# Kernel optimization log

Measured on AMD Instinct MI355X. Metric: run time of the kernel, lower is better.

The kernel has to match this reference:

```python
import jax, jax.numpy as jnp
import numpy as np
from jax.ops import segment_sum

N_NODES = 100000


def gcn_conv(x, W, b, src, dst, num_nodes):
    # PyG GCNConv: h = x @ W; add self-loops; symmetric normalization; aggregate; + bias
    h = x @ W  # [N, out]
    # add self-loops
    loops = jnp.arange(num_nodes, dtype=src.dtype)
    src_sl = jnp.concatenate([src, loops])
    dst_sl = jnp.concatenate([dst, loops])
    # degree over destination (incl. self-loops), edge weight = 1
    deg = segment_sum(jnp.ones_like(src_sl, dtype=h.dtype), dst_sl, num_segments=num_nodes)
    dinv = jnp.where(deg > 0, jax.lax.rsqrt(deg), 0.0)
    norm = dinv[src_sl] * dinv[dst_sl]  # [E+N]
    msg = h[src_sl] * norm[:, None]      # gather + scale, [E+N, out]
    out = segment_sum(msg, dst_sl, num_segments=num_nodes)  # scatter-add
    return out + b


def setup_inputs() -> dict:
    key = jax.random.key(0)
    ks = jax.random.split(key, 5)
    N, F, C = N_NODES, 64, 10
    E = 1600000
    x = jax.random.normal(ks[0], (N, F), dtype=jnp.float32)
    edge_index = jax.random.randint(ks[1], (2, E), 0, N, dtype=jnp.int64)
    W1 = jax.random.normal(ks[2], (F, 128), dtype=jnp.float32) * (1.0 / np.sqrt(F))
    b1 = jnp.zeros((128,), dtype=jnp.float32)
    W2 = jax.random.normal(ks[3], (128, 16), dtype=jnp.float32) * (1.0 / np.sqrt(128))
    b2 = jnp.zeros((16,), dtype=jnp.float32)
    Wl = jax.random.normal(ks[4], (16, C), dtype=jnp.float32) * (1.0 / np.sqrt(16))
    bl = jnp.zeros((C,), dtype=jnp.float32)
    return {"x": x, "edge_index": edge_index, "W1": W1, "b1": b1,
            "W2": W2, "b2": b2, "Wl": Wl, "bl": bl}


def reference(x, edge_index, W1, b1, W2, b2, Wl, bl):
    src, dst = edge_index[0], edge_index[1]
    h = gcn_conv(x, W1, b1, src, dst, N_NODES)
    h = jax.nn.relu(h)
    h = gcn_conv(h, W2, b2, src, dst, N_NODES)
    h = jax.nn.relu(h)
    return h @ Wl + bl
```

## Files before the change

### kernel.cpp

```cpp
#include <hip/hip_runtime.h>
#include <hip/hip_fp16.h>


#define F_IN 64
#define H1DIM 128
#define H2DIM 16
#define C_OUT 10

#define NBK 1024
#define BSZ_LOG 7
#define BNODES 128
#define CAP 2816
#define SRC_BITS 17

typedef _Float16 f16x8 __attribute__((ext_vector_type(8)));
typedef _Float16 f16x4 __attribute__((ext_vector_type(4)));
typedef float f32x4 __attribute__((ext_vector_type(4)));

__global__ __launch_bounds__(256) void setup_kernel(
        const float* __restrict__ W1, const float* __restrict__ W2,
        f16x8* __restrict__ W1p, f16x8* __restrict__ W2p,
        int* __restrict__ cur) {
    int s = blockIdx.x * 256 + threadIdx.x;
    if (s < 1024) {
        int frag = s >> 6, lane = s & 63;
        int tile = frag >> 1, kf = frag & 1;
        int c = lane & 15, g = lane >> 4;
        f16x8 v;
#pragma unroll
        for (int j = 0; j < 8; ++j)
            v[j] = (_Float16)W1[(kf * 32 + g * 8 + j) * H1DIM + tile * 16 + c];
        W1p[s] = v;
    } else if (s < 1024 + 256) {
        int s2 = s - 1024;
        int f = s2 >> 6, lane = s2 & 63;
        int c = lane & 15, g = lane >> 4;
        f16x8 v;
#pragma unroll
        for (int j = 0; j < 8; ++j)
            v[j] = (_Float16)W2[(f * 32 + g * 8 + j) * H2DIM + c];
        W2p[s2] = v;
    } else {
        int t = s - 1280;
        if (t >= 0 && t < NBK) cur[t] = t * CAP;
    }
}

__global__ __launch_bounds__(256) void bucket_scatter(
        const int* __restrict__ ei, int E, int N,
        int* __restrict__ cursor, unsigned* __restrict__ pairs) {
    __shared__ int cnt[NBK];
    __shared__ int base[NBK];
    for (int t = threadIdx.x; t < NBK; t += 256) cnt[t] = 0;
    __syncthreads();

    const int4* s4 = (const int4*)ei;
    const int4* d4 = (const int4*)(ei + E);
    int chunk4 = blockIdx.x * 1024;
    int s_[16], d_[16];
    int m = 0;
#pragma unroll
    for (int r = 0; r < 4; r++) {
        int i4 = chunk4 + r * 256 + threadIdx.x;
        if (i4 * 4 < E) {
            int4 sv = s4[i4], dv = d4[i4];
            int ss[4] = {sv.x, sv.y, sv.z, sv.w};
            int dd[4] = {dv.x, dv.y, dv.z, dv.w};
#pragma unroll
            for (int q = 0; q < 4; q++) {
                if ((unsigned)ss[q] < (unsigned)N && (unsigned)dd[q] < (unsigned)N) {
                    s_[m] = ss[q]; d_[m] = dd[q]; m++;
                }
            }
        }
    }
    for (int k = 0; k < m; k++) atomicAdd(&cnt[d_[k] >> BSZ_LOG], 1);
    __syncthreads();
    for (int t = threadIdx.x; t < NBK; t += 256) {
        int c = cnt[t];
        base[t] = c ? atomicAdd(&cursor[t], c) : 0;
        cnt[t] = 0;
    }
    __syncthreads();
    for (int k = 0; k < m; k++) {
        int b = d_[k] >> BSZ_LOG;
        int pos = base[b] + atomicAdd(&cnt[b], 1);
        if (pos < (b + 1) * CAP)
            pairs[pos] = ((unsigned)(d_[k] & (BNODES - 1)) << SRC_BITS) | (unsigned)s_[k];
    }
}

__global__ __launch_bounds__(256) void build_csr_convert(
        const unsigned* __restrict__ pairs, const int* __restrict__ cursor,
        const float* __restrict__ x, int N,
        float* __restrict__ dinv, int* __restrict__ row_beg,
        int* __restrict__ row_end, int* __restrict__ csr_src,
        __half2* __restrict__ xh2) {
    int b = blockIdx.x;
    int base_node = b << BSZ_LOG;
    int nn = min(BNODES, N - base_node);
    __shared__ unsigned lp[CAP];
    __shared__ int cnt[BNODES];
    __shared__ int sc[BNODES];
    __shared__ int cur[BNODES];
    __shared__ float sdi[BNODES];
    int tid = threadIdx.x;
    if (tid < BNODES) cnt[tid] = 0;

    int pbeg = b * CAP;
    int pend = min(cursor[b], (b + 1) * CAP);
    int np = pend - pbeg;
    for (int j = tid; j < np; j += 256) lp[j] = pairs[pbeg + j];
    __syncthreads();

    for (int j = tid; j < np; j += 256)
        atomicAdd(&cnt[lp[j] >> SRC_BITS], 1);
    __syncthreads();

    int v = (tid < BNODES) ? cnt[tid] : 0;
    if (tid < BNODES) sc[tid] = v;
    __syncthreads();
#pragma unroll
    for (int off = 1; off < BNODES; off <<= 1) {
        int t = (tid < BNODES && tid >= off) ? sc[tid - off] : 0;
        __syncthreads();
        if (tid < BNODES) sc[tid] += t;
        __syncthreads();
    }
    if (tid < nn) {
        int ro = pbeg + sc[tid] - v;
        row_beg[base_node + tid] = ro;
        row_end[base_node + tid] = ro + v;
        cur[tid] = ro;
        float di = rsqrtf((float)(v + 1));
        dinv[base_node + tid] = di;
        sdi[tid] = di;
    }
    __syncthreads();

    for (int j = tid; j < np; j += 256) {
        unsigned p = lp[j];
        int dl = p >> SRC_BITS, s = p & ((1u << SRC_BITS) - 1);
        int pos = atomicAdd(&cur[dl], 1);
        csr_src[pos] = s;
    }

    const float2* x2 = (const float2*)x;
    int total = nn * 32;
    for (int t = tid; t < total; t += 256) {
        int nl = t >> 5, l = t & 31;
        float di = sdi[nl];
        long long idx = (long long)(base_node + nl) * 32 + l;
        float2 xv = x2[idx];
        xh2[idx] = __floats2half2_rn(xv.x * di, xv.y * di);
    }
}

__global__ __launch_bounds__(256) void gather1_h2(
        const f16x8* __restrict__ xh8, const float* __restrict__ dinv,
        const int* __restrict__ row_beg, const int* __restrict__ row_end,
        const int* __restrict__ csr_src, int N, f16x8* __restrict__ agg1h8) {
    int node = (blockIdx.x * 256 + threadIdx.x) >> 3;
    if (node >= N) return;
    int p = threadIdx.x & 7;
    int beg = row_beg[node], end = row_end[node];
    f16x8 self = xh8[(size_t)node * 8 + p];
    float acc[8];
#pragma unroll
    for (int q = 0; q < 8; q++) acc[q] = (float)self[q];
    int j = beg;
    for (; j + 8 <= end; j += 8) {
        int s0 = csr_src[j],     s1 = csr_src[j + 1];
        int s2 = csr_src[j + 2], s3 = csr_src[j + 3];
        int s4 = csr_src[j + 4], s5 = csr_src[j + 5];
        int s6 = csr_src[j + 6], s7 = csr_src[j + 7];
        f16x8 v0 = xh8[(size_t)s0 * 8 + p];
        f16x8 v1 = xh8[(size_t)s1 * 8 + p];
        f16x8 v2 = xh8[(size_t)s2 * 8 + p];
        f16x8 v3 = xh8[(size_t)s3 * 8 + p];
        f16x8 v4 = xh8[(size_t)s4 * 8 + p];
        f16x8 v5 = xh8[(size_t)s5 * 8 + p];
        f16x8 v6 = xh8[(size_t)s6 * 8 + p];
        f16x8 v7 = xh8[(size_t)s7 * 8 + p];
#pragma unroll
        for (int q = 0; q < 8; q++)
            acc[q] += (((float)v0[q] + (float)v1[q]) + ((float)v2[q] + (float)v3[q]))
                    + (((float)v4[q] + (float)v5[q]) + ((float)v6[q] + (float)v7[q]));
    }
    for (; j + 4 <= end; j += 4) {
        int s0 = csr_src[j], s1 = csr_src[j + 1];
        int s2 = csr_src[j + 2], s3 = csr_src[j + 3];
        f16x8 v0 = xh8[(size_t)s0 * 8 + p];
        f16x8 v1 = xh8[(size_t)s1 * 8 + p];
        f16x8 v2 = xh8[(size_t)s2 * 8 + p];
        f16x8 v3 = xh8[(size_t)s3 * 8 + p];
#pragma unroll
        for (int q = 0; q < 8; q++)
            acc[q] += ((float)v0[q] + (float)v1[q]) + ((float)v2[q] + (float)v3[q]);
    }
    for (; j < end; ++j) {
        f16x8 v = xh8[(size_t)csr_src[j] * 8 + p];
#pragma unroll
        for (int q = 0; q < 8; q++) acc[q] += (float)v[q];
    }
    float di = dinv[node];
    f16x8 o;
#pragma unroll
    for (int q = 0; q < 8; q++) o[q] = (_Float16)(acc[q] * di);
    agg1h8[(size_t)node * 8 + p] = o;
}

__global__ __launch_bounds__(256) void dense1_mfma(
        const _Float16* __restrict__ agg, const f16x8* __restrict__ W1p,
        const f16x8* __restrict__ W2p, const float* __restrict__ b1,
        const float* __restrict__ dinv, int N, _Float16* __restrict__ z2h) {
    __shared__ float sb1[H1DIM];
    __shared__ _Float16 Hl[4][16 * H1DIM];
    if (threadIdx.x < H1DIM) sb1[threadIdx.x] = b1[threadIdx.x];
    __syncthreads();
    const int wave = threadIdx.x >> 6, lane = threadIdx.x & 63;
    const int c = lane & 15, g = lane >> 4;
    const int nodeBase = blockIdx.x * 64 + wave * 16;

    int nld = nodeBase + c; if (nld > N - 1) nld = N - 1;
    const f16x8 a0 = *(const f16x8*)(agg + (size_t)nld * 64 + g * 8);
    const f16x8 a1 = *(const f16x8*)(agg + (size_t)nld * 64 + 32 + g * 8);

    _Float16* hl = Hl[wave];
    const f32x4 zero = {0.f, 0.f, 0.f, 0.f};
#pragma unroll
    for (int t = 0; t < 8; ++t) {
        f32x4 d = __builtin_amdgcn_mfma_f32_16x16x32_f16(W1p[(t * 2 + 1) * 64 + lane], a1, zero, 0, 0, 0);
        d = __builtin_amdgcn_mfma_f32_16x16x32_f16(W1p[(t * 2 + 0) * 64 + lane], a0, d, 0, 0, 0);
        f16x4 hv;
#pragma unroll
        for (int r = 0; r < 4; ++r)
            hv[r] = (_Float16)fmaxf(d[r] + sb1[t * 16 + g * 4 + r], 0.f);
        unsigned byte = ((unsigned)c * 256 + (unsigned)t * 32 + (unsigned)g * 8) ^ ((unsigned)(c & 7) << 4);
        *(f16x4*)((char*)hl + byte) = hv;
    }

    f32x4 acc = zero;
#pragma unroll
    for (int f = 0; f < 4; ++f) {
        unsigned byte = ((unsigned)c * 256 + (unsigned)f * 64 + (unsigned)g * 16) ^ ((unsigned)(c & 7) << 4);
        f16x8 a2 = *(const f16x8*)((char*)hl + byte);
        acc = __builtin_amdgcn_mfma_f32_16x16x32_f16(a2, W2p[f * 64 + lane], acc, 0, 0, 0);
    }
#pragma unroll
    for (int r = 0; r < 4; ++r) {
        int node = nodeBase + g * 4 + r;
        if (node < N) z2h[(size_t)node * 16 + c] = (_Float16)(acc[r] * dinv[node]);
    }
}

__global__ __launch_bounds__(256) void gather2_final_v2(
        const __half2* __restrict__ z2h, const float* __restrict__ dinv,
        const int* __restrict__ row_beg, const int* __restrict__ row_end,
        const int* __restrict__ csr_src,
        const float* __restrict__ b2, const float* __restrict__ Wl,
        const float* __restrict__ bl, int N, float* __restrict__ out) {
    __shared__ float sWl[H2DIM * C_OUT];
    __shared__ float sb2[H2DIM];
    __shared__ float sbl[C_OUT];
    __shared__ float hbuf[32][17];
    int tid = threadIdx.x;
    if (tid < H2DIM * C_OUT) sWl[tid] = Wl[tid];
    if (tid < H2DIM) sb2[tid] = b2[tid];
    if (tid < C_OUT) sbl[tid] = bl[tid];
    __syncthreads();

    int node = blockIdx.x * 32 + (tid >> 3);
    int p = tid & 7;
    int ln = tid >> 3;
    if (node < N) {
        int beg = row_beg[node], end = row_end[node];
        float2 sv = __half22float2(z2h[(size_t)node * 8 + p]);
        float ax = sv.x, ay = sv.y;
        int j = beg;
        for (; j + 8 <= end; j += 8) {
            int s0 = csr_src[j],     s1 = csr_src[j + 1];
            int s2 = csr_src[j + 2], s3 = csr_src[j + 3];
            int s4 = csr_src[j + 4], s5 = csr_src[j + 5];
            int s6 = csr_src[j + 6], s7 = csr_src[j + 7];
            float2 v0 = __half22float2(z2h[(size_t)s0 * 8 + p]);
            float2 v1 = __half22float2(z2h[(size_t)s1 * 8 + p]);
            float2 v2 = __half22float2(z2h[(size_t)s2 * 8 + p]);
            float2 v3 = __half22float2(z2h[(size_t)s3 * 8 + p]);
            float2 v4 = __half22float2(z2h[(size_t)s4 * 8 + p]);
            float2 v5 = __half22float2(z2h[(size_t)s5 * 8 + p]);
            float2 v6 = __half22float2(z2h[(size_t)s6 * 8 + p]);
            float2 v7 = __half22float2(z2h[(size_t)s7 * 8 + p]);
            ax += ((v0.x + v1.x) + (v2.x + v3.x)) + ((v4.x + v5.x) + (v6.x + v7.x));
            ay += ((v0.y + v1.y) + (v2.y + v3.y)) + ((v4.y + v5.y) + (v6.y + v7.y));
        }
        for (; j + 4 <= end; j += 4) {
            int s0 = csr_src[j], s1 = csr_src[j + 1];
            int s2 = csr_src[j + 2], s3 = csr_src[j + 3];
            float2 v0 = __half22float2(z2h[(size_t)s0 * 8 + p]);
            float2 v1 = __half22float2(z2h[(size_t)s1 * 8 + p]);
            float2 v2 = __half22float2(z2h[(size_t)s2 * 8 + p]);
            float2 v3 = __half22float2(z2h[(size_t)s3 * 8 + p]);
            ax += (v0.x + v1.x) + (v2.x + v3.x);
            ay += (v0.y + v1.y) + (v2.y + v3.y);
        }
        for (; j < end; ++j) {
            float2 v = __half22float2(z2h[(size_t)csr_src[j] * 8 + p]);
            ax += v.x; ay += v.y;
        }
        float di = dinv[node];
        hbuf[ln][2 * p]     = fmaxf(ax * di + sb2[2 * p], 0.f);
        hbuf[ln][2 * p + 1] = fmaxf(ay * di + sb2[2 * p + 1], 0.f);
    }
    __syncthreads();
    if (node < N) {
        float o0 = sbl[p];
        float o1 = (p < 2) ? sbl[8 + p] : 0.f;
#pragma unroll
        for (int k = 0; k < H2DIM; k++) {
            float hk = hbuf[ln][k];
            o0 = fmaf(hk, sWl[k * C_OUT + p], o0);
            if (p < 2) o1 = fmaf(hk, sWl[k * C_OUT + 8 + p], o1);
        }
        out[(size_t)node * C_OUT + p] = o0;
        if (p < 2) out[(size_t)node * C_OUT + 8 + p] = o1;
    }
}

extern "C" void kernel_launch(void* const* d_in, const int* in_sizes, int n_in,
                              void* d_out, int out_size, void* d_ws, size_t ws_size,
                              hipStream_t stream) {
    const float* x  = (const float*)d_in[0];
    const int*   ei = (const int*)d_in[1];
    const float* W1 = (const float*)d_in[2];
    const float* b1 = (const float*)d_in[3];
    const float* W2 = (const float*)d_in[4];
    const float* b2 = (const float*)d_in[5];
    const float* Wl = (const float*)d_in[6];
    const float* bl = (const float*)d_in[7];
    float* out = (float*)d_out;

    const int N = in_sizes[0] / F_IN;
    const int E = in_sizes[1] / 2;

    size_t off = 0;
    auto carve = [&](size_t bytes) {
        void* p = (char*)d_ws + off;
        off += (bytes + 255) & ~(size_t)255;
        return p;
    };
    float*   dinv    = (float*)  carve((size_t)N * sizeof(float));
    int*     row_beg = (int*)    carve((size_t)N * sizeof(int));
    int*     row_end = (int*)    carve((size_t)N * sizeof(int));
    int*     csr_src = (int*)    carve((size_t)NBK * CAP * sizeof(int));
    __half2* xh2     = (__half2*)carve((size_t)N * 32 * sizeof(__half2));
    size_t agg_bytes = (size_t)N * 32 * sizeof(__half2);
    size_t pr_bytes  = (size_t)NBK * CAP * sizeof(unsigned);
    __half2* agg1h   = (__half2*)carve(agg_bytes > pr_bytes ? agg_bytes : pr_bytes);
    __half2* z2h     = (__half2*)carve((size_t)N * 8 * sizeof(__half2));
    int*     bcur    = (int*)    carve(NBK * sizeof(int));
    f16x8*   W1p     = (f16x8*)  carve(1024 * sizeof(f16x8));
    f16x8*   W2p     = (f16x8*)  carve(256 * sizeof(f16x8));
    unsigned* pairs = (unsigned*)agg1h;

    const int nbuckets_used = (N + BNODES - 1) >> BSZ_LOG;

    setup_kernel<<<10, 256, 0, stream>>>(W1, W2, W1p, W2p, bcur);
    bucket_scatter<<<(E + 4095) / 4096, 256, 0, stream>>>(ei, E, N, bcur, pairs);
    build_csr_convert<<<nbuckets_used, 256, 0, stream>>>(
        pairs, bcur, x, N, dinv, row_beg, row_end, csr_src, xh2);

    gather1_h2<<<((size_t)N * 8 + 255) / 256, 256, 0, stream>>>(
        (const f16x8*)xh2, dinv, row_beg, row_end, csr_src, N, (f16x8*)agg1h);
    dense1_mfma<<<(N + 63) / 64, 256, 0, stream>>>(
        (const _Float16*)agg1h, W1p, W2p, b1, dinv, N, (_Float16*)z2h);
    gather2_final_v2<<<(N + 31) / 32, 256, 0, stream>>>(
        z2h, dinv, row_beg, row_end, csr_src, b2, Wl, bl, N, out);
}
```

Before: 111.4 us.

## Fuse first-layer neighbor gather into dense MFMA kernel via LDS staging

Merges the layer-1 CSR gather kernel with the dense MFMA kernel. Each block gathers aggregated features for its 64 nodes into swizzled shared memory and then runs both matmuls from LDS, so the fp16 aggregate buffer no longer makes a round trip through global memory and one launch is removed. In exchange each thread now does two gather passes before a block barrier, and the larger shared-memory footprint may reduce occupancy for the latency-bound gather. The pairs buffer now gets its own workspace region instead of aliasing the removed aggregate buffer.

```diff
diff --git a/kernel.cpp b/kernel.cpp
--- a/kernel.cpp
+++ b/kernel.cpp
@@ -156,75 +156,80 @@
     }
 }
 
-__global__ __launch_bounds__(256) void gather1_h2(
+__global__ __launch_bounds__(256) void gather_dense_fused(
         const f16x8* __restrict__ xh8, const float* __restrict__ dinv,
         const int* __restrict__ row_beg, const int* __restrict__ row_end,
-        const int* __restrict__ csr_src, int N, f16x8* __restrict__ agg1h8) {
-    int node = (blockIdx.x * 256 + threadIdx.x) >> 3;
-    if (node >= N) return;
-    int p = threadIdx.x & 7;
-    int beg = row_beg[node], end = row_end[node];
-    f16x8 self = xh8[(size_t)node * 8 + p];
-    float acc[8];
-#pragma unroll
-    for (int q = 0; q < 8; q++) acc[q] = (float)self[q];
-    int j = beg;
-    for (; j + 8 <= end; j += 8) {
-        int s0 = csr_src[j],     s1 = csr_src[j + 1];
-        int s2 = csr_src[j + 2], s3 = csr_src[j + 3];
-        int s4 = csr_src[j + 4], s5 = csr_src[j + 5];
-        int s6 = csr_src[j + 6], s7 = csr_src[j + 7];
-        f16x8 v0 = xh8[(size_t)s0 * 8 + p];
-        f16x8 v1 = xh8[(size_t)s1 * 8 + p];
-        f16x8 v2 = xh8[(size_t)s2 * 8 + p];
-        f16x8 v3 = xh8[(size_t)s3 * 8 + p];
-        f16x8 v4 = xh8[(size_t)s4 * 8 + p];
-        f16x8 v5 = xh8[(size_t)s5 * 8 + p];
-        f16x8 v6 = xh8[(size_t)s6 * 8 + p];
-        f16x8 v7 = xh8[(size_t)s7 * 8 + p];
-#pragma unroll
-        for (int q = 0; q < 8; q++)
-            acc[q] += (((float)v0[q] + (float)v1[q]) + ((float)v2[q] + (float)v3[q]))
-                    + (((float)v4[q] + (float)v5[q]) + ((float)v6[q] + (float)v7[q]));
-    }
-    for (; j + 4 <= end; j += 4) {
-        int s0 = csr_src[j], s1 = csr_src[j + 1];
-        int s2 = csr_src[j + 2], s3 = csr_src[j + 3];
-        f16x8 v0 = xh8[(size_t)s0 * 8 + p];
-        f16x8 v1 = xh8[(size_t)s1 * 8 + p];
-        f16x8 v2 = xh8[(size_t)s2 * 8 + p];
-        f16x8 v3 = xh8[(size_t)s3 * 8 + p];
-#pragma unroll
-        for (int q = 0; q < 8; q++)
-            acc[q] += ((float)v0[q] + (float)v1[q]) + ((float)v2[q] + (float)v3[q]);
-    }
-    for (; j < end; ++j) {
-        f16x8 v = xh8[(size_t)csr_src[j] * 8 + p];
-#pragma unroll
-        for (int q = 0; q < 8; q++) acc[q] += (float)v[q];
-    }
-    float di = dinv[node];
-    f16x8 o;
-#pragma unroll
-    for (int q = 0; q < 8; q++) o[q] = (_Float16)(acc[q] * di);
-    agg1h8[(size_t)node * 8 + p] = o;
-}
-
-__global__ __launch_bounds__(256) void dense1_mfma(
-        const _Float16* __restrict__ agg, const f16x8* __restrict__ W1p,
-        const f16x8* __restrict__ W2p, const float* __restrict__ b1,
-        const float* __restrict__ dinv, int N, _Float16* __restrict__ z2h) {
+        const int* __restrict__ csr_src,
+        const f16x8* __restrict__ W1p, const f16x8* __restrict__ W2p,
+        const float* __restrict__ b1, int N, _Float16* __restrict__ z2h) {
+    __shared__ _Float16 Ax[64 * 64];
     __shared__ float sb1[H1DIM];
     __shared__ _Float16 Hl[4][16 * H1DIM];
-    if (threadIdx.x < H1DIM) sb1[threadIdx.x] = b1[threadIdx.x];
-    __syncthreads();
-    const int wave = threadIdx.x >> 6, lane = threadIdx.x & 63;
+    const int tid = threadIdx.x;
+    if (tid < H1DIM) sb1[tid] = b1[tid];
+
+    const int p = tid & 7;
+#pragma unroll
+    for (int pass = 0; pass < 2; ++pass) {
+        int nl = (tid >> 3) + pass * 32;
+        int node = blockIdx.x * 64 + nl;
+        f16x8 o = {};
+        if (node < N) {
+            int beg = row_beg[node], end = row_end[node];
+            f16x8 self = xh8[(size_t)node * 8 + p];
+            float acc[8];
+#pragma unroll
+            for (int q = 0; q < 8; q++) acc[q] = (float)self[q];
+            int j = beg;
+            for (; j + 8 <= end; j += 8) {
+                int s0 = csr_src[j],     s1 = csr_src[j + 1];
+                int s2 = csr_src[j + 2], s3 = csr_src[j + 3];
+                int s4 = csr_src[j + 4], s5 = csr_src[j + 5];
+                int s6 = csr_src[j + 6], s7 = csr_src[j + 7];
+                f16x8 v0 = xh8[(size_t)s0 * 8 + p];
+                f16x8 v1 = xh8[(size_t)s1 * 8 + p];
+                f16x8 v2 = xh8[(size_t)s2 * 8 + p];
+                f16x8 v3 = xh8[(size_t)s3 * 8 + p];
+                f16x8 v4 = xh8[(size_t)s4 * 8 + p];
+                f16x8 v5 = xh8[(size_t)s5 * 8 + p];
+                f16x8 v6 = xh8[(size_t)s6 * 8 + p];
+                f16x8 v7 = xh8[(size_t)s7 * 8 + p];
+#pragma unroll
+                for (int q = 0; q < 8; q++)
+                    acc[q] += (((float)v0[q] + (float)v1[q]) + ((float)v2[q] + (float)v3[q]))
+                            + (((float)v4[q] + (float)v5[q]) + ((float)v6[q] + (float)v7[q]));
+            }
+            for (; j + 4 <= end; j += 4) {
+                int s0 = csr_src[j], s1 = csr_src[j + 1];
+                int s2 = csr_src[j + 2], s3 = csr_src[j + 3];
+                f16x8 v0 = xh8[(size_t)s0 * 8 + p];
+                f16x8 v1 = xh8[(size_t)s1 * 8 + p];
+                f16x8 v2 = xh8[(size_t)s2 * 8 + p];
+                f16x8 v3 = xh8[(size_t)s3 * 8 + p];
+#pragma unroll
+                for (int q = 0; q < 8; q++)
+                    acc[q] += ((float)v0[q] + (float)v1[q]) + ((float)v2[q] + (float)v3[q]);
+            }
+            for (; j < end; ++j) {
+                f16x8 v = xh8[(size_t)csr_src[j] * 8 + p];
+#pragma unroll
+                for (int q = 0; q < 8; q++) acc[q] += (float)v[q];
+            }
+            float di = dinv[node];
+#pragma unroll
+            for (int q = 0; q < 8; q++) o[q] = (_Float16)(acc[q] * di);
+        }
+        *(f16x8*)(&Ax[nl * 64 + ((p ^ (nl & 7)) << 3)]) = o;
+    }
+    __syncthreads();
+
+    const int wave = tid >> 6, lane = tid & 63;
     const int c = lane & 15, g = lane >> 4;
     const int nodeBase = blockIdx.x * 64 + wave * 16;
-
-    int nld = nodeBase + c; if (nld > N - 1) nld = N - 1;
-    const f16x8 a0 = *(const f16x8*)(agg + (size_t)nld * 64 + g * 8);
-    const f16x8 a1 = *(const f16x8*)(agg + (size_t)nld * 64 + 32 + g * 8);
+    const int nl16 = wave * 16 + c;
+
+    const f16x8 a0 = *(const f16x8*)(&Ax[nl16 * 64 + ((g ^ (nl16 & 7)) << 3)]);
+    const f16x8 a1 = *(const f16x8*)(&Ax[nl16 * 64 + (((g + 4) ^ (nl16 & 7)) << 3)]);
 
     _Float16* hl = Hl[wave];
     const f32x4 zero = {0.f, 0.f, 0.f, 0.f};
@@ -240,17 +245,17 @@
         *(f16x4*)((char*)hl + byte) = hv;
     }
 
-    f32x4 acc = zero;
+    f32x4 acc2 = zero;
 #pragma unroll
     for (int f = 0; f < 4; ++f) {
         unsigned byte = ((unsigned)c * 256 + (unsigned)f * 64 + (unsigned)g * 16) ^ ((unsigned)(c & 7) << 4);
         f16x8 a2 = *(const f16x8*)((char*)hl + byte);
-        acc = __builtin_amdgcn_mfma_f32_16x16x32_f16(a2, W2p[f * 64 + lane], acc, 0, 0, 0);
+        acc2 = __builtin_amdgcn_mfma_f32_16x16x32_f16(a2, W2p[f * 64 + lane], acc2, 0, 0, 0);
     }
 #pragma unroll
     for (int r = 0; r < 4; ++r) {
         int node = nodeBase + g * 4 + r;
-        if (node < N) z2h[(size_t)node * 16 + c] = (_Float16)(acc[r] * dinv[node]);
+        if (node < N) z2h[(size_t)node * 16 + c] = (_Float16)(acc2[r] * dinv[node]);
     }
 }
 
@@ -354,26 +359,20 @@
     int*     row_end = (int*)    carve((size_t)N * sizeof(int));
     int*     csr_src = (int*)    carve((size_t)NBK * CAP * sizeof(int));
     __half2* xh2     = (__half2*)carve((size_t)N * 32 * sizeof(__half2));
-    size_t agg_bytes = (size_t)N * 32 * sizeof(__half2);
-    size_t pr_bytes  = (size_t)NBK * CAP * sizeof(unsigned);
-    __half2* agg1h   = (__half2*)carve(agg_bytes > pr_bytes ? agg_bytes : pr_bytes);
+    unsigned* pairs  = (unsigned*)carve((size_t)NBK * CAP * sizeof(unsigned));
     __half2* z2h     = (__half2*)carve((size_t)N * 8 * sizeof(__half2));
     int*     bcur    = (int*)    carve(NBK * sizeof(int));
     f16x8*   W1p     = (f16x8*)  carve(1024 * sizeof(f16x8));
     f16x8*   W2p     = (f16x8*)  carve(256 * sizeof(f16x8));
-    unsigned* pairs = (unsigned*)agg1h;
-
-    const int nbuckets_used = (N + BNODES - 1) >> BSZ_LOG;
 
     setup_kernel<<<10, 256, 0, stream>>>(W1, W2, W1p, W2p, bcur);
     bucket_scatter<<<(E + 4095) / 4096, 256, 0, stream>>>(ei, E, N, bcur, pairs);
-    build_csr_convert<<<nbuckets_used, 256, 0, stream>>>(
+    build_csr_convert<<<(N + BNODES - 1) >> BSZ_LOG, 256, 0, stream>>>(
         pairs, bcur, x, N, dinv, row_beg, row_end, csr_src, xh2);
 
-    gather1_h2<<<((size_t)N * 8 + 255) / 256, 256, 0, stream>>>(
-        (const f16x8*)xh2, dinv, row_beg, row_end, csr_src, N, (f16x8*)agg1h);
-    dense1_mfma<<<(N + 63) / 64, 256, 0, stream>>>(
-        (const _Float16*)agg1h, W1p, W2p, b1, dinv, N, (_Float16*)z2h);
+    gather_dense_fused<<<(N + 63) / 64, 256, 0, stream>>>(
+        (const f16x8*)xh2, dinv, row_beg, row_end, csr_src,
+        W1p, W2p, b1, N, (_Float16*)z2h);
     gather2_final_v2<<<(N + 31) / 32, 256, 0, stream>>>(
         z2h, dinv, row_beg, row_end, csr_src, b2, Wl, bl, N, out);
 }
```

New measurement: 111.0 us. About the same (-0.4%).
